# Optimization experiments

Hardware: AMD Instinct MI355X
Metric: run time of the kernel (lower is better)

Reference implementation:

```python
import jax, jax.numpy as jnp
import numpy as np

N_NODES = 100000
N_EDGES = 1600000
DIM = 64
N_GRAPHS = 1000


def setup_inputs() -> dict:
    key = jax.random.key(0)
    ks = jax.random.split(key, 6)
    s = 1.0 / np.sqrt(DIM)
    x = jax.random.normal(ks[0], (N_NODES, DIM), dtype=jnp.float32)
    edge_index = jax.random.randint(ks[1], (2, N_EDGES), 0, N_NODES, dtype=jnp.int64)
    batch = jnp.sort(jax.random.randint(ks[2], (N_NODES,), 0, N_GRAPHS, dtype=jnp.int64))
    W1 = jax.random.normal(ks[3], (DIM, DIM), dtype=jnp.float32) * s
    b1 = jnp.zeros((DIM,), jnp.float32)
    W2 = jax.random.normal(ks[4], (DIM, DIM), dtype=jnp.float32) * s
    b2 = jnp.zeros((DIM,), jnp.float32)
    return {"x": x, "W1": W1, "b1": b1, "W2": W2, "b2": b2,
            "edge_index": edge_index, "batch": batch}


def reference(x, W1, b1, W2, b2, edge_index, batch):
    n = x.shape[0]
    loop = jnp.arange(n, dtype=edge_index.dtype)
    src = jnp.concatenate([edge_index[0], loop])  # [E+N] with self-loops
    dst = jnp.concatenate([edge_index[1], loop])
    # symmetric GCN normalization: deg^{-1/2}[src] * deg^{-1/2}[dst]
    deg = jax.ops.segment_sum(jnp.ones(src.shape[0], x.dtype), dst, num_segments=n)
    dinv = jax.lax.rsqrt(jnp.maximum(deg, 1.0))  # deg >= 1 due to self-loops
    norm = (dinv[src] * dinv[dst])[:, None]      # [E+N, 1]

    def gcn(h, W, b):
        h = h @ W                                  # transform first (smaller dim path)
        msg = h[src] * norm                        # gather + normalize
        return jax.ops.segment_sum(msg, dst, num_segments=n) + b

    h = jax.nn.relu(gcn(x, W1, b1))
    # dropout: eval mode -> identity
    h = jax.nn.relu(gcn(h, W2, b2))

    counts = jax.ops.segment_sum(jnp.ones((n,), x.dtype), batch, num_segments=N_GRAPHS)
    pooled = jax.ops.segment_sum(h, batch, num_segments=N_GRAPHS)
    return pooled / jnp.maximum(counts, 1.0)[:, None]
```

## Files before the change

kernel.cpp:

```cpp
#include <hip/hip_runtime.h>
#include <hip/hip_fp16.h>

#define DIM 64
#define BIN_SHIFT 7
#define BINSZ 128
#define MAXBINS 1024
#define PB 512
#define PB_LOG 9

typedef __attribute__((ext_vector_type(2))) float floatx2;
typedef __attribute__((ext_vector_type(4))) float f32x4;
typedef __attribute__((ext_vector_type(8))) _Float16 f16x8;
typedef __attribute__((ext_vector_type(4))) _Float16 f16x4;


__global__ __launch_bounds__(256) void k_hist(const int* __restrict__ dst,
                                              int* __restrict__ C, int E, int NB) {
    __shared__ int h[MAXBINS];
    for (int i = threadIdx.x; i < NB; i += 256) h[i] = 0;
    __syncthreads();
    int per = (E + PB - 1) / PB;
    int e0 = blockIdx.x * per;
    int e1 = e0 + per; if (e1 > E) e1 = E;
    for (int e = e0 + (int)threadIdx.x; e < e1; e += 256)
        atomicAdd(&h[dst[e] >> BIN_SHIFT], 1);
    __syncthreads();
    for (int i = threadIdx.x; i < NB; i += 256)
        C[blockIdx.x * NB + i] = h[i];
}


__global__ __launch_bounds__(1024) void k_scanA(const int* __restrict__ C,
                                                int* __restrict__ S,
                                                int* __restrict__ bsums, int NB, int M) {
    __shared__ int sh[1024];
    int tid = threadIdx.x;
    int j0 = blockIdx.x * 4096 + tid * 4;
    int v[4]; int sum = 0;
#pragma unroll
    for (int t = 0; t < 4; ++t) {
        int j = j0 + t; int x = 0;
        if (j < M) { int bin = j >> PB_LOG, blk = j & (PB - 1); x = C[blk * NB + bin]; }
        v[t] = sum; sum += x;
    }
    sh[tid] = sum;
    __syncthreads();
#pragma unroll
    for (int d = 1; d < 1024; d <<= 1) {
        int t = (tid >= d) ? sh[tid - d] : 0;
        __syncthreads();
        sh[tid] += t;
        __syncthreads();
    }
    int excl = sh[tid] - sum;
#pragma unroll
    for (int t = 0; t < 4; ++t) {
        int j = j0 + t;
        if (j < M) S[j] = excl + v[t];
    }
    if (tid == 1023) bsums[blockIdx.x] = sh[1023];
}


__global__ __launch_bounds__(1024) void k_scanB(int* __restrict__ bsums, int nb) {
    __shared__ int s[1024];
    int tid = threadIdx.x;
    int v = (tid < nb) ? bsums[tid] : 0;
    s[tid] = v;
    __syncthreads();
#pragma unroll
    for (int d = 1; d < 1024; d <<= 1) {
        int t = (tid >= d) ? s[tid - d] : 0;
        __syncthreads();
        s[tid] += t;
        __syncthreads();
    }
    if (tid < nb) bsums[tid] = s[tid] - v;
}


__global__ __launch_bounds__(256) void k_bucket(const int* __restrict__ src,
                                                const int* __restrict__ dst,
                                                const int* __restrict__ S,
                                                const int* __restrict__ bsums,
                                                int* __restrict__ bkt, int E, int NB) {
    __shared__ int lcur[MAXBINS];
    int blk = blockIdx.x;
    for (int i = threadIdx.x; i < NB; i += 256) {
        int j = i * PB + blk;
        lcur[i] = S[j] + bsums[j >> 12];
    }
    __syncthreads();
    int per = (E + PB - 1) / PB;
    int e0 = blk * per;
    int e1 = e0 + per; if (e1 > E) e1 = E;
    for (int e = e0 + (int)threadIdx.x; e < e1; e += 256) {
        int d = dst[e];
        int pos = atomicAdd(&lcur[d >> BIN_SHIFT], 1);
        bkt[pos] = src[e] | ((d & (BINSZ - 1)) << 24);
    }
}


__global__ __launch_bounds__(256) void k_binsort(const int* __restrict__ bkt,
                                                 const int* __restrict__ S,
                                                 const int* __restrict__ bsums,
                                                 int* __restrict__ csr,
                                                 int* __restrict__ off,
                                                 float* __restrict__ dinv,
                                                 const int* __restrict__ batch,
                                                 int* __restrict__ goff,
                                                 float* __restrict__ outz,
                                                 int N, int G, int E, int NB) {
    __shared__ int cnt[BINSZ], bas[BINSZ], cur[BINSZ];
    __shared__ int wsum[4];
    int tid = threadIdx.x;
    int b = blockIdx.x;
    for (int i = b * 256 + tid; i < G * DIM; i += NB * 256) outz[i] = 0.f;
    int j0 = b << PB_LOG;
    int s0 = S[j0] + bsums[j0 >> 12];
    int s1 = E;
    if (b + 1 < NB) { int j1 = (b + 1) << PB_LOG; s1 = S[j1] + bsums[j1 >> 12]; }
    if (tid < BINSZ) { cnt[tid] = 0; cur[tid] = 0; }
    __syncthreads();
    for (int i = s0 + tid; i < s1; i += 256)
        atomicAdd(&cnt[(bkt[i] >> 24) & (BINSZ - 1)], 1);
    __syncthreads();
    int my = (tid < BINSZ) ? cnt[tid] : 0;
    int lane = tid & 63, wv = tid >> 6;
    int x = my;
#pragma unroll
    for (int d = 1; d < 64; d <<= 1) {
        int t = __shfl_up(x, d);
        if (lane >= d) x += t;
    }
    if (lane == 63) wsum[wv] = x;
    __syncthreads();
    int prefix = 0;
    for (int w = 0; w < wv; ++w) prefix += wsum[w];
    int ex = x + prefix - my;
    if (tid < BINSZ) {
        bas[tid] = ex;
        int v = (b << BIN_SHIFT) + tid;
        if (v < N) {
            off[v] = s0 + ex;
            dinv[v] = rsqrtf((float)(my + 1));
            if (v == N - 1) off[N] = E;
            int bb = batch[v];
            int prev = (v == 0) ? -1 : batch[v - 1];
            for (int g = prev + 1; g <= bb; ++g) goff[g] = v;
            if (v == N - 1)
                for (int g = bb + 1; g <= G; ++g) goff[g] = N;
        }
    }
    __syncthreads();
    for (int i = s0 + tid; i < s1; i += 256) {
        int p = bkt[i];
        int lo = (p >> 24) & (BINSZ - 1);
        int li = atomicAdd(&cur[lo], 1);
        csr[s0 + bas[lo] + li] = p & 0xFFFFFF;
    }
}


__global__ __launch_bounds__(256) void k_gemm(const float* __restrict__ X,
                                              const float* __restrict__ W,
                                              const float* __restrict__ dinv,
                                              unsigned int* __restrict__ Y8, int N) {
    __shared__ float Os[16 * 68];
    int tid = threadIdx.x;
    int lane = tid & 63, w = tid >> 6;
    int m = lane & 15, g = lane >> 4;
    int row0 = blockIdx.x * 16;
    int row = row0 + m;

    f16x8 B0, B1;
    {
        int n = (w << 4) + m;
        const float* wp = W + (g << 3) * 64 + n;
#pragma unroll
        for (int j = 0; j < 8; ++j) B0[j] = (_Float16)wp[j * 64];
        wp += 32 * 64;
#pragma unroll
        for (int j = 0; j < 8; ++j) B1[j] = (_Float16)wp[j * 64];
    }
    f16x8 A0, A1;
    {
        float4 u0 = make_float4(0.f, 0.f, 0.f, 0.f), u1 = u0, u2 = u0, u3 = u0;
        if (row < N) {
            const float* xp = X + (size_t)row * DIM + (g << 3);
            u0 = *(const float4*)(xp);
            u1 = *(const float4*)(xp + 4);
            u2 = *(const float4*)(xp + 32);
            u3 = *(const float4*)(xp + 36);
        }
        A0[0] = (_Float16)u0.x; A0[1] = (_Float16)u0.y; A0[2] = (_Float16)u0.z; A0[3] = (_Float16)u0.w;
        A0[4] = (_Float16)u1.x; A0[5] = (_Float16)u1.y; A0[6] = (_Float16)u1.z; A0[7] = (_Float16)u1.w;
        A1[0] = (_Float16)u2.x; A1[1] = (_Float16)u2.y; A1[2] = (_Float16)u2.z; A1[3] = (_Float16)u2.w;
        A1[4] = (_Float16)u3.x; A1[5] = (_Float16)u3.y; A1[6] = (_Float16)u3.z; A1[7] = (_Float16)u3.w;
    }
    f32x4 acc = {0.f, 0.f, 0.f, 0.f};
    acc = __builtin_amdgcn_mfma_f32_16x16x32_f16(A0, B0, acc, 0, 0, 0);
    acc = __builtin_amdgcn_mfma_f32_16x16x32_f16(A1, B1, acc, 0, 0, 0);
#pragma unroll
    for (int j = 0; j < 4; ++j)
        Os[((g << 2) + j) * 68 + (w << 4) + m] = acc[j];
    __syncthreads();

    int r = tid >> 4, c = tid & 15;
    int orow = row0 + r;
    if (orow < N) {
        float4 o = *(const float4*)(Os + r * 68 + (c << 2));
        float s = dinv[orow];
        int p = 0;
        p = __builtin_amdgcn_cvt_pk_fp8_f32(o.x * s, o.y * s, p, false);
        p = __builtin_amdgcn_cvt_pk_fp8_f32(o.z * s, o.w * s, p, true);
        Y8[(size_t)orow * 16 + c] = (unsigned int)p;
    } else if (orow == N) {
        Y8[(size_t)orow * 16 + c] = 0u;
    }
}


__device__ __forceinline__ float4 gather_rows(const unsigned int* __restrict__ hs8,
                                              const int* __restrict__ csr,
                                              int k0, int k1, int v, int l, int gw4,
                                              int N) {
    int p = l >> 3, s = l & 7;
    float4 alo = make_float4(0.f, 0.f, 0.f, 0.f);
    float4 ahi = make_float4(0.f, 0.f, 0.f, 0.f);
    if (p == 0) {
        uint2 u = *(const uint2*)(hs8 + (((unsigned)v << 4) | (s << 1)));
        floatx2 f0 = __builtin_amdgcn_cvt_pk_f32_fp8((int)u.x, false);
        floatx2 f1 = __builtin_amdgcn_cvt_pk_f32_fp8((int)u.x, true);
        floatx2 f2 = __builtin_amdgcn_cvt_pk_f32_fp8((int)u.y, false);
        floatx2 f3 = __builtin_amdgcn_cvt_pk_f32_fp8((int)u.y, true);
        alo = make_float4(f0.x, f0.y, f1.x, f1.y);
        ahi = make_float4(f2.x, f2.y, f3.x, f3.y);
    }
    int kb = k0;
    int idx = N;
    if (kb < k1) idx = (l < k1 - kb) ? csr[kb + l] : N;
    while (kb < k1) {
        int nkb = kb + 16;
        uint2 uu[8];
#pragma unroll
        for (int t = 0; t < 8; ++t) {
            int e = __shfl(idx, gw4 + (t << 1) + p);
            uu[t] = *(const uint2*)(hs8 + (((unsigned)e << 4) | (s << 1)));
        }
        if (nkb < k1) idx = (l < k1 - nkb) ? csr[nkb + l] : N;
#pragma unroll
        for (int t = 0; t < 8; ++t) {
            floatx2 f0 = __builtin_amdgcn_cvt_pk_f32_fp8((int)uu[t].x, false);
            floatx2 f1 = __builtin_amdgcn_cvt_pk_f32_fp8((int)uu[t].x, true);
            floatx2 f2 = __builtin_amdgcn_cvt_pk_f32_fp8((int)uu[t].y, false);
            floatx2 f3 = __builtin_amdgcn_cvt_pk_f32_fp8((int)uu[t].y, true);
            alo.x += f0.x; alo.y += f0.y; alo.z += f1.x; alo.w += f1.y;
            ahi.x += f2.x; ahi.y += f2.y; ahi.z += f3.x; ahi.w += f3.y;
        }
        kb = nkb;
    }
    alo.x += __shfl_xor(alo.x, 8); alo.y += __shfl_xor(alo.y, 8);
    alo.z += __shfl_xor(alo.z, 8); alo.w += __shfl_xor(alo.w, 8);
    ahi.x += __shfl_xor(ahi.x, 8); ahi.y += __shfl_xor(ahi.y, 8);
    ahi.z += __shfl_xor(ahi.z, 8); ahi.w += __shfl_xor(ahi.w, 8);
    return p ? ahi : alo;
}


__global__ __launch_bounds__(256) void k_gather_gemm(const unsigned int* __restrict__ hs8,
                                                     const int* __restrict__ csr,
                                                     const int* __restrict__ off,
                                                     const float* __restrict__ dinv,
                                                     const float* __restrict__ bias,
                                                     const float* __restrict__ W,
                                                     unsigned int* __restrict__ hs_out,
                                                     int N) {
    __shared__ _Float16 Xs[16 * 72];
    __shared__ float Os[16 * 68];
    int tid = threadIdx.x;
    int r = tid >> 4, l = tid & 15;
    int c4g = ((l & 7) << 1) | (l >> 3);
    int lane = tid & 63, w = tid >> 6;
    int m = lane & 15, g = lane >> 4;
    int gw4 = (r & 3) << 4;
    int v = blockIdx.x * 16 + r;

    f16x8 B0, B1;
    {
        int n = (w << 4) + m;
        const float* wp = W + (g << 3) * 64 + n;
#pragma unroll
        for (int j = 0; j < 8; ++j) B0[j] = (_Float16)wp[j * 64];
        wp += 32 * 64;
#pragma unroll
        for (int j = 0; j < 8; ++j) B1[j] = (_Float16)wp[j * 64];
    }
    if (blockIdx.x == 0 && tid < 16)
        hs_out[(size_t)N * 16 + tid] = 0u;

    float dv = 0.f;
    float4 h = make_float4(0.f, 0.f, 0.f, 0.f);
    if (v < N) {
        dv = dinv[v];
        float4 bv = ((const float4*)bias)[c4g];
        float4 acc = gather_rows(hs8, csr, off[v], off[v + 1], v, l, gw4, N);
        h.x = fmaxf(acc.x * dv + bv.x, 0.f);
        h.y = fmaxf(acc.y * dv + bv.y, 0.f);
        h.z = fmaxf(acc.z * dv + bv.z, 0.f);
        h.w = fmaxf(acc.w * dv + bv.w, 0.f);
    }
    {
        f16x4 hv;
        hv[0] = (_Float16)h.x; hv[1] = (_Float16)h.y;
        hv[2] = (_Float16)h.z; hv[3] = (_Float16)h.w;
        *(f16x4*)(Xs + r * 72 + (c4g << 2)) = hv;
    }
    __syncthreads();

    f16x8 A0 = *(const f16x8*)(Xs + m * 72 + (g << 3));
    f16x8 A1 = *(const f16x8*)(Xs + m * 72 + 32 + (g << 3));
    f32x4 acc2 = {0.f, 0.f, 0.f, 0.f};
    acc2 = __builtin_amdgcn_mfma_f32_16x16x32_f16(A0, B0, acc2, 0, 0, 0);
    acc2 = __builtin_amdgcn_mfma_f32_16x16x32_f16(A1, B1, acc2, 0, 0, 0);
#pragma unroll
    for (int j = 0; j < 4; ++j)
        Os[((g << 2) + j) * 68 + (w << 4) + m] = acc2[j];
    __syncthreads();

    if (v < N) {
        float4 o = *(const float4*)(Os + r * 68 + (c4g << 2));
        int p = 0;
        p = __builtin_amdgcn_cvt_pk_fp8_f32(o.x * dv, o.y * dv, p, false);
        p = __builtin_amdgcn_cvt_pk_fp8_f32(o.z * dv, o.w * dv, p, true);
        hs_out[(size_t)v * 16 + c4g] = (unsigned int)p;
    }
}


__global__ __launch_bounds__(256) void k_gather_pool(const unsigned int* __restrict__ hs8,
                                                     const int* __restrict__ csr,
                                                     const int* __restrict__ off,
                                                     const float* __restrict__ dinv,
                                                     const float* __restrict__ bias,
                                                     const int* __restrict__ batch,
                                                     const int* __restrict__ goff,
                                                     float* __restrict__ out, int N) {
    __shared__ float vals[16][68];
    __shared__ int gid[16];
    int tid = threadIdx.x;
    int r = tid >> 4, l = tid & 15;
    int c4g = ((l & 7) << 1) | (l >> 3);
    int gw4 = (r & 3) << 4;
    int v = blockIdx.x * 16 + r;

    float4 val = make_float4(0.f, 0.f, 0.f, 0.f);
    int g = -1;
    if (v < N) {
        g = batch[v];
        float dv = dinv[v];
        float4 bv = ((const float4*)bias)[c4g];
        float4 acc = gather_rows(hs8, csr, off[v], off[v + 1], v, l, gw4, N);
        float inv = 1.0f / (float)(goff[g + 1] - goff[g]);
        val.x = fmaxf(acc.x * dv + bv.x, 0.f) * inv;
        val.y = fmaxf(acc.y * dv + bv.y, 0.f) * inv;
        val.z = fmaxf(acc.z * dv + bv.z, 0.f) * inv;
        val.w = fmaxf(acc.w * dv + bv.w, 0.f) * inv;
    }
    *(float4*)(&vals[r][c4g << 2]) = val;
    if (l == 0) gid[r] = g;
    __syncthreads();

    if (v < N) {
        bool leader = (r == 0) || (gid[r - 1] != g);
        if (leader) {
            float4 sacc = val;
            for (int rr = r + 1; rr < 16 && gid[rr] == g; ++rr) {
                float4 t = *(const float4*)(&vals[rr][c4g << 2]);
                sacc.x += t.x; sacc.y += t.y; sacc.z += t.z; sacc.w += t.w;
            }
            float* op = out + (size_t)g * DIM + (c4g << 2);
            atomicAdd(op + 0, sacc.x);
            atomicAdd(op + 1, sacc.y);
            atomicAdd(op + 2, sacc.z);
            atomicAdd(op + 3, sacc.w);
        }
    }
}


static inline int cdiv(int a, int b) { return (a + b - 1) / b; }

extern "C" void kernel_launch(void* const* d_in, const int* in_sizes, int n_in,
                              void* d_out, int out_size, void* d_ws, size_t ws_size,
                              hipStream_t stream) {
    const float* x   = (const float*)d_in[0];
    const float* W1  = (const float*)d_in[1];
    const float* b1  = (const float*)d_in[2];
    const float* W2  = (const float*)d_in[3];
    const float* b2  = (const float*)d_in[4];
    const int*   ei  = (const int*)d_in[5];
    const int*   bat = (const int*)d_in[6];

    const int N = in_sizes[0] / DIM;
    const int E = in_sizes[5] / 2;
    const int G = out_size / DIM;
    const int NB = cdiv(N, BINSZ);
    const int M  = NB * PB;
    const int* src = ei;
    const int* dst = ei + E;
    float* out = (float*)d_out;

    __half* hs1    = (__half*)d_ws;
    __half* hs2    = hs1 + (size_t)(N + 1) * DIM;
    __half* spare  = hs2 + (size_t)(N + 1) * DIM;
    float*  dinv   = (float*)(spare + (size_t)N * DIM);
    int*    off    = (int*)(dinv + N);
    int*    goff   = off + (N + 1);
    int*    C      = goff + (G + 1);
    int*    S      = C + (size_t)PB * NB;
    int*    bsums  = S + (size_t)PB * NB;
    int*    csr    = bsums + 1024;
    int*    bkt    = (int*)hs1;

    k_hist<<<PB, 256, 0, stream>>>(dst, C, E, NB);
    int nb2 = cdiv(M, 4096);
    k_scanA<<<nb2, 1024, 0, stream>>>(C, S, bsums, NB, M);
    k_scanB<<<1, 1024, 0, stream>>>(bsums, nb2);
    k_bucket<<<PB, 256, 0, stream>>>(src, dst, S, bsums, bkt, E, NB);
    k_binsort<<<NB, 256, 0, stream>>>(bkt, S, bsums, csr, off, dinv, bat, goff,
                                      out, N, G, E, NB);

    k_gemm<<<cdiv(N + 1, 16), 256, 0, stream>>>(x, W1, dinv, (unsigned int*)hs1, N);

    k_gather_gemm<<<cdiv(N, 16), 256, 0, stream>>>((const unsigned int*)hs1, csr, off,
                                                   dinv, b1, W2, (unsigned int*)hs2, N);

    k_gather_pool<<<cdiv(N, 16), 256, 0, stream>>>((const unsigned int*)hs2, csr, off,
                                                   dinv, b2, bat, goff, out, N);
}
```

Before: 197.8 us.

## Split fp8 feature tables into column halves mapped to separate XCD groups

The fp8 node-feature table is split into two 32-column halves stored as separate arrays. Gather blocks are assigned so that blocks on XCDs 0-3 read one half and XCDs 4-7 read the other, which shrinks the per-XCD gather working set so it fits better in each XCD's L2. The fused gather+GEMM kernel is broken into a gather kernel that writes fp16 aggregates and a separate GEMM kernel, which adds an extra fp16 round trip through memory and one more launch. The gather loop now uses 8 lanes per row with a single 32-bit load per lane and two accumulators.

```diff
diff --git a/kernel.cpp b/kernel.cpp
--- a/kernel.cpp
+++ b/kernel.cpp
@@ -166,7 +166,8 @@
 __global__ __launch_bounds__(256) void k_gemm(const float* __restrict__ X,
                                               const float* __restrict__ W,
                                               const float* __restrict__ dinv,
-                                              unsigned int* __restrict__ Y8, int N) {
+                                              unsigned int* __restrict__ YA,
+                                              unsigned int* __restrict__ YB, int N) {
     __shared__ float Os[16 * 68];
     int tid = threadIdx.x;
     int lane = tid & 63, w = tid >> 6;
@@ -209,83 +210,97 @@
 
     int r = tid >> 4, c = tid & 15;
     int orow = row0 + r;
+    unsigned int* T = (c < 8) ? YA : YB;
+    int ci = c & 7;
     if (orow < N) {
         float4 o = *(const float4*)(Os + r * 68 + (c << 2));
         float s = dinv[orow];
         int p = 0;
         p = __builtin_amdgcn_cvt_pk_fp8_f32(o.x * s, o.y * s, p, false);
         p = __builtin_amdgcn_cvt_pk_fp8_f32(o.z * s, o.w * s, p, true);
-        Y8[(size_t)orow * 16 + c] = (unsigned int)p;
+        T[(size_t)orow * 8 + ci] = (unsigned int)p;
     } else if (orow == N) {
-        Y8[(size_t)orow * 16 + c] = 0u;
-    }
-}
-
-
-__device__ __forceinline__ float4 gather_rows(const unsigned int* __restrict__ hs8,
-                                              const int* __restrict__ csr,
-                                              int k0, int k1, int v, int l, int gw4,
-                                              int N) {
-    int p = l >> 3, s = l & 7;
-    float4 alo = make_float4(0.f, 0.f, 0.f, 0.f);
-    float4 ahi = make_float4(0.f, 0.f, 0.f, 0.f);
-    if (p == 0) {
-        uint2 u = *(const uint2*)(hs8 + (((unsigned)v << 4) | (s << 1)));
-        floatx2 f0 = __builtin_amdgcn_cvt_pk_f32_fp8((int)u.x, false);
-        floatx2 f1 = __builtin_amdgcn_cvt_pk_f32_fp8((int)u.x, true);
-        floatx2 f2 = __builtin_amdgcn_cvt_pk_f32_fp8((int)u.y, false);
-        floatx2 f3 = __builtin_amdgcn_cvt_pk_f32_fp8((int)u.y, true);
-        alo = make_float4(f0.x, f0.y, f1.x, f1.y);
-        ahi = make_float4(f2.x, f2.y, f3.x, f3.y);
+        T[(size_t)orow * 8 + ci] = 0u;
+    }
+}
+
+
+__device__ __forceinline__ float4 gather_rows8(const unsigned int* __restrict__ tab,
+                                               const int* __restrict__ csr,
+                                               int k0, int k1, int v, int l3, int gbase,
+                                               int N) {
+    float4 a, b;
+    {
+        unsigned int u = tab[((unsigned)v << 3) | l3];
+        floatx2 f0 = __builtin_amdgcn_cvt_pk_f32_fp8((int)u, false);
+        floatx2 f1 = __builtin_amdgcn_cvt_pk_f32_fp8((int)u, true);
+        a = make_float4(f0.x, f0.y, f1.x, f1.y);
+        b = make_float4(0.f, 0.f, 0.f, 0.f);
     }
     int kb = k0;
-    int idx = N;
-    if (kb < k1) idx = (l < k1 - kb) ? csr[kb + l] : N;
+    int idx = (k0 + l3 < k1) ? csr[k0 + l3] : N;
     while (kb < k1) {
-        int nkb = kb + 16;
-        uint2 uu[8];
+        int nkb = kb + 8;
+        unsigned int uu[8];
 #pragma unroll
         for (int t = 0; t < 8; ++t) {
-            int e = __shfl(idx, gw4 + (t << 1) + p);
-            uu[t] = *(const uint2*)(hs8 + (((unsigned)e << 4) | (s << 1)));
-        }
-        if (nkb < k1) idx = (l < k1 - nkb) ? csr[nkb + l] : N;
-#pragma unroll
-        for (int t = 0; t < 8; ++t) {
-            floatx2 f0 = __builtin_amdgcn_cvt_pk_f32_fp8((int)uu[t].x, false);
-            floatx2 f1 = __builtin_amdgcn_cvt_pk_f32_fp8((int)uu[t].x, true);
-            floatx2 f2 = __builtin_amdgcn_cvt_pk_f32_fp8((int)uu[t].y, false);
-            floatx2 f3 = __builtin_amdgcn_cvt_pk_f32_fp8((int)uu[t].y, true);
-            alo.x += f0.x; alo.y += f0.y; alo.z += f1.x; alo.w += f1.y;
-            ahi.x += f2.x; ahi.y += f2.y; ahi.z += f3.x; ahi.w += f3.y;
+            int e = __shfl(idx, gbase + t);
+            uu[t] = tab[((unsigned)e << 3) | l3];
+        }
+        idx = (nkb + l3 < k1) ? csr[nkb + l3] : N;
+#pragma unroll
+        for (int t = 0; t < 8; t += 2) {
+            floatx2 f0 = __builtin_amdgcn_cvt_pk_f32_fp8((int)uu[t], false);
+            floatx2 f1 = __builtin_amdgcn_cvt_pk_f32_fp8((int)uu[t], true);
+            floatx2 g0 = __builtin_amdgcn_cvt_pk_f32_fp8((int)uu[t + 1], false);
+            floatx2 g1 = __builtin_amdgcn_cvt_pk_f32_fp8((int)uu[t + 1], true);
+            a.x += f0.x; a.y += f0.y; a.z += f1.x; a.w += f1.y;
+            b.x += g0.x; b.y += g0.y; b.z += g1.x; b.w += g1.y;
         }
         kb = nkb;
     }
-    alo.x += __shfl_xor(alo.x, 8); alo.y += __shfl_xor(alo.y, 8);
-    alo.z += __shfl_xor(alo.z, 8); alo.w += __shfl_xor(alo.w, 8);
-    ahi.x += __shfl_xor(ahi.x, 8); ahi.y += __shfl_xor(ahi.y, 8);
-    ahi.z += __shfl_xor(ahi.z, 8); ahi.w += __shfl_xor(ahi.w, 8);
-    return p ? ahi : alo;
-}
-
-
-__global__ __launch_bounds__(256) void k_gather_gemm(const unsigned int* __restrict__ hs8,
+    return make_float4(a.x + b.x, a.y + b.y, a.z + b.z, a.w + b.w);
+}
+
+
+__global__ __launch_bounds__(256) void k_gather_half(const unsigned int* __restrict__ hsA,
+                                                     const unsigned int* __restrict__ hsB,
                                                      const int* __restrict__ csr,
                                                      const int* __restrict__ off,
-                                                     const float* __restrict__ dinv,
-                                                     const float* __restrict__ bias,
-                                                     const float* __restrict__ W,
-                                                     unsigned int* __restrict__ hs_out,
-                                                     int N) {
-    __shared__ _Float16 Xs[16 * 72];
+                                                     __half* __restrict__ agg, int N,
+                                                     int NBLK32) {
+    int bb = blockIdx.x;
+    int xcd = bb & 7, half = xcd >> 2, l4 = xcd & 3;
+    int nb = (bb >> 3) * 4 + l4;
+    if (nb >= NBLK32) return;
+    int tid = threadIdx.x;
+    int r = tid >> 3, l3 = tid & 7;
+    int gbase = (tid & 63) & ~7;
+    int v = nb * 32 + r;
+    if (v >= N) return;
+    const unsigned int* tab = half ? hsB : hsA;
+    float4 acc = gather_rows8(tab, csr, off[v], off[v + 1], v, l3, gbase, N);
+    __half2 p0 = __floats2half2_rn(acc.x, acc.y);
+    __half2 p1 = __floats2half2_rn(acc.z, acc.w);
+    uint2 u;
+    u.x = *(unsigned int*)&p0;
+    u.y = *(unsigned int*)&p1;
+    ((uint2*)agg)[(size_t)v * 16 + half * 8 + l3] = u;
+}
+
+
+__global__ __launch_bounds__(256) void k_gemm2(const __half* __restrict__ agg,
+                                               const float* __restrict__ W,
+                                               const float* __restrict__ b1,
+                                               const float* __restrict__ dinv,
+                                               unsigned int* __restrict__ YA,
+                                               unsigned int* __restrict__ YB, int N) {
     __shared__ float Os[16 * 68];
     int tid = threadIdx.x;
-    int r = tid >> 4, l = tid & 15;
-    int c4g = ((l & 7) << 1) | (l >> 3);
     int lane = tid & 63, w = tid >> 6;
     int m = lane & 15, g = lane >> 4;
-    int gw4 = (r & 3) << 4;
-    int v = blockIdx.x * 16 + r;
+    int row0 = blockIdx.x * 16;
+    int row = row0 + m;
 
     f16x8 B0, B1;
     {
@@ -297,90 +312,97 @@
 #pragma unroll
         for (int j = 0; j < 8; ++j) B1[j] = (_Float16)wp[j * 64];
     }
-    if (blockIdx.x == 0 && tid < 16)
-        hs_out[(size_t)N * 16 + tid] = 0u;
-
-    float dv = 0.f;
-    float4 h = make_float4(0.f, 0.f, 0.f, 0.f);
-    if (v < N) {
-        dv = dinv[v];
-        float4 bv = ((const float4*)bias)[c4g];
-        float4 acc = gather_rows(hs8, csr, off[v], off[v + 1], v, l, gw4, N);
-        h.x = fmaxf(acc.x * dv + bv.x, 0.f);
-        h.y = fmaxf(acc.y * dv + bv.y, 0.f);
-        h.z = fmaxf(acc.z * dv + bv.z, 0.f);
-        h.w = fmaxf(acc.w * dv + bv.w, 0.f);
-    }
-    {
-        f16x4 hv;
-        hv[0] = (_Float16)h.x; hv[1] = (_Float16)h.y;
-        hv[2] = (_Float16)h.z; hv[3] = (_Float16)h.w;
-        *(f16x4*)(Xs + r * 72 + (c4g << 2)) = hv;
-    }
-    __syncthreads();
-
-    f16x8 A0 = *(const f16x8*)(Xs + m * 72 + (g << 3));
-    f16x8 A1 = *(const f16x8*)(Xs + m * 72 + 32 + (g << 3));
-    f32x4 acc2 = {0.f, 0.f, 0.f, 0.f};
-    acc2 = __builtin_amdgcn_mfma_f32_16x16x32_f16(A0, B0, acc2, 0, 0, 0);
-    acc2 = __builtin_amdgcn_mfma_f32_16x16x32_f16(A1, B1, acc2, 0, 0, 0);
+    f16x8 A0, A1;
+    if (row < N) {
+        float dv = dinv[row];
+        const __half2* ap2 = (const __half2*)(agg + (size_t)row * 64 + (g << 3));
+#pragma unroll
+        for (int j = 0; j < 4; ++j) {
+            float2 f = __half22float2(ap2[j]);
+            float2 fb = __half22float2(ap2[j + 16]);
+            int k0 = (g << 3) + 2 * j;
+            A0[2 * j]     = (_Float16)fmaxf(f.x * dv + b1[k0], 0.f);
+            A0[2 * j + 1] = (_Float16)fmaxf(f.y * dv + b1[k0 + 1], 0.f);
+            A1[2 * j]     = (_Float16)fmaxf(fb.x * dv + b1[32 + k0], 0.f);
+            A1[2 * j + 1] = (_Float16)fmaxf(fb.y * dv + b1[32 + k0 + 1], 0.f);
+        }
+    } else {
+#pragma unroll
+        for (int j = 0; j < 8; ++j) { A0[j] = (_Float16)0.f; A1[j] = (_Float16)0.f; }
+    }
+    f32x4 acc = {0.f, 0.f, 0.f, 0.f};
+    acc = __builtin_amdgcn_mfma_f32_16x16x32_f16(A0, B0, acc, 0, 0, 0);
+    acc = __builtin_amdgcn_mfma_f32_16x16x32_f16(A1, B1, acc, 0, 0, 0);
 #pragma unroll
     for (int j = 0; j < 4; ++j)
-        Os[((g << 2) + j) * 68 + (w << 4) + m] = acc2[j];
-    __syncthreads();
-
-    if (v < N) {
-        float4 o = *(const float4*)(Os + r * 68 + (c4g << 2));
+        Os[((g << 2) + j) * 68 + (w << 4) + m] = acc[j];
+    __syncthreads();
+
+    int r = tid >> 4, c = tid & 15;
+    int orow = row0 + r;
+    unsigned int* T = (c < 8) ? YA : YB;
+    int ci = c & 7;
+    if (orow < N) {
+        float4 o = *(const float4*)(Os + r * 68 + (c << 2));
+        float s = dinv[orow];
         int p = 0;
-        p = __builtin_amdgcn_cvt_pk_fp8_f32(o.x * dv, o.y * dv, p, false);
-        p = __builtin_amdgcn_cvt_pk_fp8_f32(o.z * dv, o.w * dv, p, true);
-        hs_out[(size_t)v * 16 + c4g] = (unsigned int)p;
-    }
-}
-
-
-__global__ __launch_bounds__(256) void k_gather_pool(const unsigned int* __restrict__ hs8,
+        p = __builtin_amdgcn_cvt_pk_fp8_f32(o.x * s, o.y * s, p, false);
+        p = __builtin_amdgcn_cvt_pk_fp8_f32(o.z * s, o.w * s, p, true);
+        T[(size_t)orow * 8 + ci] = (unsigned int)p;
+    } else if (orow == N) {
+        T[(size_t)orow * 8 + ci] = 0u;
+    }
+}
+
+
+__global__ __launch_bounds__(256) void k_gather_pool(const unsigned int* __restrict__ hsA,
+                                                     const unsigned int* __restrict__ hsB,
                                                      const int* __restrict__ csr,
                                                      const int* __restrict__ off,
                                                      const float* __restrict__ dinv,
                                                      const float* __restrict__ bias,
                                                      const int* __restrict__ batch,
                                                      const int* __restrict__ goff,
-                                                     float* __restrict__ out, int N) {
-    __shared__ float vals[16][68];
-    __shared__ int gid[16];
-    int tid = threadIdx.x;
-    int r = tid >> 4, l = tid & 15;
-    int c4g = ((l & 7) << 1) | (l >> 3);
-    int gw4 = (r & 3) << 4;
-    int v = blockIdx.x * 16 + r;
+                                                     float* __restrict__ out, int N,
+                                                     int NBLK32) {
+    __shared__ float vals[32][36];
+    __shared__ int gid[32];
+    int bb = blockIdx.x;
+    int xcd = bb & 7, half = xcd >> 2, l4 = xcd & 3;
+    int nb = (bb >> 3) * 4 + l4;
+    if (nb >= NBLK32) return;
+    int tid = threadIdx.x;
+    int r = tid >> 3, l3 = tid & 7;
+    int gbase = (tid & 63) & ~7;
+    int v = nb * 32 + r;
 
     float4 val = make_float4(0.f, 0.f, 0.f, 0.f);
     int g = -1;
     if (v < N) {
         g = batch[v];
         float dv = dinv[v];
-        float4 bv = ((const float4*)bias)[c4g];
-        float4 acc = gather_rows(hs8, csr, off[v], off[v + 1], v, l, gw4, N);
+        const unsigned int* tab = half ? hsB : hsA;
+        float4 bv = ((const float4*)bias)[half * 8 + l3];
+        float4 acc = gather_rows8(tab, csr, off[v], off[v + 1], v, l3, gbase, N);
         float inv = 1.0f / (float)(goff[g + 1] - goff[g]);
         val.x = fmaxf(acc.x * dv + bv.x, 0.f) * inv;
         val.y = fmaxf(acc.y * dv + bv.y, 0.f) * inv;
         val.z = fmaxf(acc.z * dv + bv.z, 0.f) * inv;
         val.w = fmaxf(acc.w * dv + bv.w, 0.f) * inv;
     }
-    *(float4*)(&vals[r][c4g << 2]) = val;
-    if (l == 0) gid[r] = g;
+    *(float4*)(&vals[r][l3 << 2]) = val;
+    if (l3 == 0) gid[r] = g;
     __syncthreads();
 
     if (v < N) {
         bool leader = (r == 0) || (gid[r - 1] != g);
         if (leader) {
             float4 sacc = val;
-            for (int rr = r + 1; rr < 16 && gid[rr] == g; ++rr) {
-                float4 t = *(const float4*)(&vals[rr][c4g << 2]);
+            for (int rr = r + 1; rr < 32 && gid[rr] == g; ++rr) {
+                float4 t = *(const float4*)(&vals[rr][l3 << 2]);
                 sacc.x += t.x; sacc.y += t.y; sacc.z += t.z; sacc.w += t.w;
             }
-            float* op = out + (size_t)g * DIM + (c4g << 2);
+            float* op = out + (size_t)g * DIM + half * 32 + (l3 << 2);
             atomicAdd(op + 0, sacc.x);
             atomicAdd(op + 1, sacc.y);
             atomicAdd(op + 2, sacc.z);
@@ -412,17 +434,19 @@
     const int* dst = ei + E;
     float* out = (float*)d_out;
 
-    __half* hs1    = (__half*)d_ws;
-    __half* hs2    = hs1 + (size_t)(N + 1) * DIM;
-    __half* spare  = hs2 + (size_t)(N + 1) * DIM;
-    float*  dinv   = (float*)(spare + (size_t)N * DIM);
+    unsigned int* hs1A = (unsigned int*)d_ws;
+    unsigned int* hs1B = hs1A + (size_t)(N + 1) * 8;
+    unsigned int* hs2A = hs1B + (size_t)(N + 1) * 8;
+    unsigned int* hs2B = hs2A + (size_t)(N + 1) * 8;
+    __half* agg1   = (__half*)(hs2B + (size_t)(N + 1) * 8);
+    float*  dinv   = (float*)(agg1 + (size_t)N * DIM);
     int*    off    = (int*)(dinv + N);
     int*    goff   = off + (N + 1);
     int*    C      = goff + (G + 1);
     int*    S      = C + (size_t)PB * NB;
     int*    bsums  = S + (size_t)PB * NB;
     int*    csr    = bsums + 1024;
-    int*    bkt    = (int*)hs1;
+    int*    bkt    = (int*)agg1;
 
     k_hist<<<PB, 256, 0, stream>>>(dst, C, E, NB);
     int nb2 = cdiv(M, 4096);
@@ -432,11 +456,15 @@
     k_binsort<<<NB, 256, 0, stream>>>(bkt, S, bsums, csr, off, dinv, bat, goff,
                                       out, N, G, E, NB);
 
-    k_gemm<<<cdiv(N + 1, 16), 256, 0, stream>>>(x, W1, dinv, (unsigned int*)hs1, N);
-
-    k_gather_gemm<<<cdiv(N, 16), 256, 0, stream>>>((const unsigned int*)hs1, csr, off,
-                                                   dinv, b1, W2, (unsigned int*)hs2, N);
-
-    k_gather_pool<<<cdiv(N, 16), 256, 0, stream>>>((const unsigned int*)hs2, csr, off,
-                                                   dinv, b2, bat, goff, out, N);
-}
+    const int NBLK32 = cdiv(N, 32);
+    const int GGRID  = 8 * cdiv(NBLK32, 4);
+
+    k_gemm<<<cdiv(N + 1, 16), 256, 0, stream>>>(x, W1, dinv, hs1A, hs1B, N);
+
+    k_gather_half<<<GGRID, 256, 0, stream>>>(hs1A, hs1B, csr, off, agg1, N, NBLK32);
+
+    k_gemm2<<<cdiv(N + 1, 16), 256, 0, stream>>>(agg1, W2, b1, dinv, hs2A, hs2B, N);
+
+    k_gather_pool<<<GGRID, 256, 0, stream>>>(hs2A, hs2B, csr, off, dinv, b2, bat,
+                                             goff, out, N, NBLK32);
+}
```

Result: slower. 205.7 us (+4.0%).
